# Kernel tuning notes

Hardware: AMD Instinct MI355X
Metric: run time of the kernel (lower is better)

The kernel has to match this reference:

```python
import jax, jax.numpy as jnp
import numpy as np

ALPHA = 1.5
BETA = 45.0
LAMDA = 0.5
B = 8192   # batch_size
D = 128    # feature dim (hardcoded in original via zeros((1,128)))
V = 4      # number of views stacked in fj
EPS = 1e-12  # F.normalize eps


def _l2norm_rows(x):
    n = jnp.sqrt(jnp.sum(x * x, axis=-1, keepdims=True))
    return x / jnp.maximum(n, EPS)


def setup_inputs() -> dict:
    key = jax.random.key(0)
    k1, k2 = jax.random.split(key)
    fi = jax.random.normal(k1, (B, D), dtype=jnp.float32)
    fj = jax.random.normal(k2, (V, B, D), dtype=jnp.float32)
    # L2-normalize embeddings so exp(beta*(SVM - lamda)) stays finite (beta=45)
    fi = _l2norm_rows(fi)
    fj = _l2norm_rows(fj)
    return {"fi": fi, "fj": fj, "b": V}


def avg_svm(fi, fj):
    # Original: per-row softmax-weighted average of fj rows, renormalized,
    # dotted with fi row, averaged over the batch.
    A = fi @ fj.T                      # [B, B] pairwise logits
    W = jax.nn.softmax(A, axis=1)      # softmax over j (alphalist / sumofalpha)
    Vw = W @ fj                        # [B, D] softmax-weighted averages
    Vn = _l2norm_rows(Vw)              # F.normalize(p=2, dim=1)
    return jnp.mean(jnp.sum(fi * Vn, axis=1))  # mean_i fi[i] . Vn[i]


def reference(fi, fj, b):
    b = int(b)
    # SMM1 is recomputed identically every outer iteration in the original;
    # compute once and multiply the per-iteration term by (b-1).
    smm1 = avg_svm(fi, fi)
    if b > 2:
        # inner loop: SMM2sum is a running (cumulative) sum over j=1..b-2,
        # and exp(beta*(SMM2sum - lamda)) is added at every step.
        s_vals = jnp.stack([avg_svm(fi, fj[j]) for j in range(1, b - 1)])
        cum = jnp.cumsum(s_vals)
        ssum = jnp.sum(jnp.exp(BETA * (cum - LAMDA)))
    else:
        ssum = jnp.exp(BETA * (avg_svm(fi, fj) - LAMDA))
    term = (1.0 / ALPHA) * jnp.log1p(jnp.exp(-ALPHA * (smm1 - LAMDA))) \
         + (1.0 / BETA) * jnp.log1p(ssum)
    loss = (b - 1) * term
    return jnp.squeeze(loss)
```

## Files before the change

### kernel.cpp

```cpp
#include <hip/hip_runtime.h>

#define BDIM 8192
#define DDIM 128

typedef __attribute__((ext_vector_type(4))) float floatx4;
typedef __attribute__((ext_vector_type(4))) int   intx4;
typedef __attribute__((ext_vector_type(8))) int   intx8;

#define SLAB (BDIM * DDIM)
#define G8_OFF 64
#define G8T_OFF (64 + 3 * SLAB)

__device__ inline void load_lds16(const void* g, void* l) {
    __builtin_amdgcn_global_load_lds(
        (const __attribute__((address_space(1))) unsigned int*)g,
        (__attribute__((address_space(3))) unsigned int*)l, 16, 0, 0);
}

__device__ inline intx8 ld_pair(const char* base, int c0) {
    union { intx8 v; intx4 h[2]; } u;
    u.h[0] = *(const intx4*)(base + c0 * 16);
    u.h[1] = *(const intx4*)(base + (c0 ^ 1) * 16);
    return u.v;
}

__global__ __launch_bounds__(256)
void prep_kernel(const float* __restrict__ fi, const float* __restrict__ fj,
                 unsigned char* __restrict__ g8, unsigned char* __restrict__ g8T,
                 float* __restrict__ acc)
{
    const int p = blockIdx.y;
    const int kblock = blockIdx.x;
    const int rbase = kblock * 32;
    const int tid = threadIdx.x;
    if (p == 0 && kblock == 0 && tid < 8) acc[tid] = 0.f;
    const float* src = (p == 0) ? fi : (fj + (size_t)p * SLAB);

    __shared__ __align__(16) unsigned char T8[32][144];

    {
        const int row = tid >> 3, c = tid & 7;
        const float* sp = src + (size_t)(rbase + row) * DDIM + c * 16;
        float4 f0 = ((const float4*)sp)[0];
        float4 f1 = ((const float4*)sp)[1];
        float4 f2 = ((const float4*)sp)[2];
        float4 f3 = ((const float4*)sp)[3];
        alignas(16) int w[4];
        w[0] = __builtin_amdgcn_cvt_pk_fp8_f32(f0.x, f0.y, 0, false);
        w[0] = __builtin_amdgcn_cvt_pk_fp8_f32(f0.z, f0.w, w[0], true);
        w[1] = __builtin_amdgcn_cvt_pk_fp8_f32(f1.x, f1.y, 0, false);
        w[1] = __builtin_amdgcn_cvt_pk_fp8_f32(f1.z, f1.w, w[1], true);
        w[2] = __builtin_amdgcn_cvt_pk_fp8_f32(f2.x, f2.y, 0, false);
        w[2] = __builtin_amdgcn_cvt_pk_fp8_f32(f2.z, f2.w, w[2], true);
        w[3] = __builtin_amdgcn_cvt_pk_fp8_f32(f3.x, f3.y, 0, false);
        w[3] = __builtin_amdgcn_cvt_pk_fp8_f32(f3.z, f3.w, w[3], true);
        int4 v = *(int4*)w;
        *(int4*)(g8 + (size_t)p * SLAB + (size_t)(rbase + row) * DDIM + c * 16) = v;
        *(int4*)(&T8[row][c * 16]) = v;
    }
    __syncthreads();
    {
        const int d = tid >> 1, half = tid & 1;
        alignas(16) unsigned char bb[16];
        #pragma unroll
        for (int i = 0; i < 16; ++i) bb[i] = T8[half * 16 + i][d];
        *(int4*)(g8T + (size_t)p * SLAB + (size_t)kblock * 4096 + d * 32 + half * 16) =
            *(int4*)bb;
    }
}

__global__ __launch_bounds__(256, 3)
void flash_kernel(const float* __restrict__ fi,
                  const unsigned char* __restrict__ g8,
                  const unsigned char* __restrict__ g8T,
                  float* __restrict__ acc)
{
    const int b = blockIdx.x;
    const int gp = (b & 7) * 96 + (b >> 3);
    const int p = gp >> 8;
    const int qbase = (gp & 255) * 32;
    const int tid = threadIdx.x;
    const int wave = tid >> 6, lane = tid & 63;
    const int quad = lane >> 4, col = lane & 15;

    __shared__ __align__(16) char smem[37888];
    #define KOFF 0
    #define VOFF 16384
    #define POFF 32768
    #define DOFF 36864
    #define NOFF 37376

    const unsigned char* g8p  = g8  + (size_t)p * SLAB;
    const unsigned char* g8Tp = g8T + (size_t)p * SLAB;

    intx8 qf[2];
    #pragma unroll
    for (int qt = 0; qt < 2; ++qt) {
        const intx4* qp = (const intx4*)(g8 + (size_t)(qbase + qt * 16 + col) * DDIM +
                                         quad * 32);
        union { intx8 v; intx4 h[2]; } u;
        u.h[0] = qp[0];
        u.h[1] = qp[1];
        qf[qt] = u.v;
    }

    floatx4 O[2][2];
    #pragma unroll
    for (int qt = 0; qt < 2; ++qt)
        #pragma unroll
        for (int j = 0; j < 2; ++j)
            O[qt][j] = (floatx4){0.f, 0.f, 0.f, 0.f};

    auto stageK = [&](int kb) {
        #pragma unroll
        for (int i = 0; i < 4; ++i) {
            int s = i * 64 + lane;
            int key = s >> 3, cp = s & 7;
            int c = cp ^ (key & 7);
            const unsigned char* gp8 = g8p +
                (size_t)(kb + wave * 32 + key) * DDIM + c * 16;
            load_lds16(gp8, smem + KOFF + wave * 4096 + i * 1024);
        }
    };
    auto stageV = [&](int kb) {
        #pragma unroll
        for (int i = 0; i < 4; ++i) {
            int s = wave * 256 + i * 64 + lane;
            int d = s >> 3, cp = s & 7;
            int c = cp ^ (d & 7);
            const unsigned char* gp8 = g8Tp +
                (size_t)((kb >> 5) + (c >> 1)) * 4096 + d * 32 + (c & 1) * 16;
            load_lds16(gp8, smem + VOFF + wave * 4096 + i * 1024);
        }
    };

    stageK(0);
    stageV(0);
    __syncthreads();

    for (int k = 0; k < 64; ++k) {
        floatx4 S[2][2];
        #pragma unroll
        for (int kt = 0; kt < 2; ++kt) {
            const int key = kt * 16 + col;
            const int c0 = (quad * 2) ^ (key & 7);
            intx8 kf = ld_pair(smem + KOFF + wave * 4096 + key * 128, c0);
            #pragma unroll
            for (int qt = 0; qt < 2; ++qt)
                S[kt][qt] = __builtin_amdgcn_mfma_scale_f32_16x16x128_f8f6f4(
                    kf, qf[qt], (floatx4){0.f, 0.f, 0.f, 0.f},
                    0, 0,
                    0, 127,
                    0, 127);
        }

        if (k + 1 < 64) stageK((k + 1) * 128);

        #pragma unroll
        for (int kt = 0; kt < 2; ++kt)
            #pragma unroll
            for (int qt = 0; qt < 2; ++qt) {
                int v = __builtin_amdgcn_cvt_pk_fp8_f32(
                    __expf(fminf(S[kt][qt][0], 4.f)),
                    __expf(fminf(S[kt][qt][1], 4.f)), 0, false);
                v = __builtin_amdgcn_cvt_pk_fp8_f32(
                    __expf(fminf(S[kt][qt][2], 4.f)),
                    __expf(fminf(S[kt][qt][3], 4.f)), v, true);
                const int q = qt * 16 + col;
                *(int*)(smem + POFF + q * 128 +
                        (((wave * 2 + kt) ^ (q & 7)) * 16) + quad * 4) = v;
            }

        __syncthreads();

        {
            intx8 vf[2];
            #pragma unroll
            for (int j = 0; j < 2; ++j) {
                const int d = (wave * 2 + j) * 16 + col;
                vf[j] = ld_pair(smem + VOFF + d * 128, (quad * 2) ^ (d & 7));
            }
            #pragma unroll
            for (int qt = 0; qt < 2; ++qt) {
                const int q = qt * 16 + col;
                intx8 pf = ld_pair(smem + POFF + q * 128, (quad * 2) ^ (q & 7));
                #pragma unroll
                for (int j = 0; j < 2; ++j)
                    O[qt][j] = __builtin_amdgcn_mfma_scale_f32_16x16x128_f8f6f4(
                        pf, vf[j], O[qt][j], 0, 0, 0, 127, 0, 127);
            }
        }

        __syncthreads();

        if (k + 1 < 64) stageV((k + 1) * 128);
    }

    float* pdot = (float*)(smem + DOFF);
    float* pnrm = (float*)(smem + NOFF);
    #pragma unroll
    for (int qt = 0; qt < 2; ++qt)
        #pragma unroll
        for (int r = 0; r < 4; ++r) {
            const int q = qt * 16 + quad * 4 + r;
            float dot = 0.f, nr = 0.f;
            #pragma unroll
            for (int j = 0; j < 2; ++j) {
                float o = O[qt][j][r];
                float fq = fi[(size_t)(qbase + q) * DDIM + (wave * 2 + j) * 16 + col];
                dot += fq * o;
                nr += o * o;
            }
            #pragma unroll
            for (int m = 1; m < 16; m <<= 1) {
                dot += __shfl_xor(dot, m, 64);
                nr  += __shfl_xor(nr,  m, 64);
            }
            if (col == 0) {
                pdot[wave * 32 + q] = dot;
                pnrm[wave * 32 + q] = nr;
            }
        }
    __syncthreads();
    if (tid < 32) {
        const int q = tid;
        float D = pdot[q] + pdot[32 + q] + pdot[64 + q] + pdot[96 + q];
        float N = pnrm[q] + pnrm[32 + q] + pnrm[64 + q] + pnrm[96 + q];
        float val = D * rsqrtf(fmaxf(N, 1e-30f));
        #pragma unroll
        for (int m = 1; m < 32; m <<= 1) val += __shfl_xor(val, m, 64);
        if (tid == 0) atomicAdd(&acc[p], val);
    }
}

__global__ void final_kernel(const float* __restrict__ acc, float* __restrict__ out)
{
    if (threadIdx.x == 0 && blockIdx.x == 0) {
        const double s0 = (double)acc[0] / (double)BDIM;
        const double s1 = (double)acc[1] / (double)BDIM;
        const double s2 = (double)acc[2] / (double)BDIM;
        const double t1 = (1.0 / 1.5) * log1p(exp(-1.5 * (s0 - 0.5)));
        const double ssum = exp(45.0 * (s1 - 0.5)) + exp(45.0 * (s1 + s2 - 0.5));
        const double t2 = (1.0 / 45.0) * log1p(ssum);
        out[0] = (float)(3.0 * (t1 + t2));
    }
}

extern "C" void kernel_launch(void* const* d_in, const int* in_sizes, int n_in,
                              void* d_out, int out_size, void* d_ws, size_t ws_size,
                              hipStream_t stream)
{
    const float* fi = (const float*)d_in[0];
    const float* fj = (const float*)d_in[1];

    float* acc = (float*)d_ws;
    unsigned char* g8  = (unsigned char*)d_ws + G8_OFF;
    unsigned char* g8T = (unsigned char*)d_ws + G8T_OFF;

    prep_kernel <<<dim3(BDIM / 32, 3), 256, 0, stream>>>(fi, fj, g8, g8T, acc);
    flash_kernel<<<dim3(768), 256, 0, stream>>>(fi, g8, g8T, acc);
    final_kernel<<<1, 64, 0, stream>>>(acc, (float*)d_out);
}
```

Before: 158.1 us.

## Share K/V tiles across three query groups per 768-thread block with double buffering

The flash kernel is restructured into 256 blocks of 12 waves, with three query groups of four waves each sharing the same K/V tiles staged in LDS. Up to two problem slabs can be staged when a block's queries straddle a slab boundary. K and V are double-buffered and prefetched one iteration ahead using raw s_waitcnt/s_barrier, cutting global-to-LDS traffic and one barrier per iteration. It also drops the fminf clamp before exp. The cost is a large LDS footprint (140 KB), one block per CU, and more complex synchronisation.

```diff
diff --git a/kernel.cpp b/kernel.cpp
--- a/kernel.cpp
+++ b/kernel.cpp
@@ -69,34 +69,41 @@
     }
 }
 
-__global__ __launch_bounds__(256, 3)
+__global__ __launch_bounds__(768)
 void flash_kernel(const float* __restrict__ fi,
                   const unsigned char* __restrict__ g8,
                   const unsigned char* __restrict__ g8T,
                   float* __restrict__ acc)
 {
-    const int b = blockIdx.x;
-    const int gp = (b & 7) * 96 + (b >> 3);
-    const int p = gp >> 8;
-    const int qbase = (gp & 255) * 32;
+    const int bid = blockIdx.x;
+    const int gp = (bid & 7) * 32 + (bid >> 3);
     const int tid = threadIdx.x;
     const int wave = tid >> 6, lane = tid & 63;
+    const int g = wave >> 2, kw = wave & 3;
     const int quad = lane >> 4, col = lane & 15;
 
-    __shared__ __align__(16) char smem[37888];
+    const int qglob = gp * 96 + g * 32;
+    const int pg    = qglob >> 13;
+    const int qloc  = qglob & 8191;
+    const int pA    = (gp * 96) >> 13;
+    const int pB    = (gp * 96 + 64) >> 13;
+    const int need2 = (pB != pA) ? 1 : 0;
+    const int selg  = (pg != pA) ? 1 : 0;
+
+    __shared__ __align__(16) char smem[143360];
     #define KOFF 0
-    #define VOFF 16384
-    #define POFF 32768
-    #define DOFF 36864
-    #define NOFF 37376
-
-    const unsigned char* g8p  = g8  + (size_t)p * SLAB;
-    const unsigned char* g8Tp = g8T + (size_t)p * SLAB;
+    #define VOFF 65536
+    #define POFF 131072
+
+    const unsigned char* kA8 = g8  + (size_t)pA * SLAB;
+    const unsigned char* kB8 = g8  + (size_t)pB * SLAB;
+    const unsigned char* vAT = g8T + (size_t)pA * SLAB;
+    const unsigned char* vBT = g8T + (size_t)pB * SLAB;
 
     intx8 qf[2];
     #pragma unroll
     for (int qt = 0; qt < 2; ++qt) {
-        const intx4* qp = (const intx4*)(g8 + (size_t)(qbase + qt * 16 + col) * DDIM +
+        const intx4* qp = (const intx4*)(g8 + (size_t)(qloc + qt * 16 + col) * DDIM +
                                          quad * 32);
         union { intx8 v; intx4 h[2]; } u;
         u.h[0] = qp[0];
@@ -111,79 +118,91 @@
         for (int j = 0; j < 2; ++j)
             O[qt][j] = (floatx4){0.f, 0.f, 0.f, 0.f};
 
-    auto stageK = [&](int kb) {
-        #pragma unroll
-        for (int i = 0; i < 4; ++i) {
-            int s = i * 64 + lane;
-            int key = s >> 3, cp = s & 7;
-            int c = cp ^ (key & 7);
-            const unsigned char* gp8 = g8p +
-                (size_t)(kb + wave * 32 + key) * DDIM + c * 16;
-            load_lds16(gp8, smem + KOFF + wave * 4096 + i * 1024);
+    auto stageK = [&](int kb, int buf) {
+        for (int s = 0; s <= need2; ++s) {
+            const unsigned char* src = s ? kB8 : kA8;
+            #pragma unroll
+            for (int i = 0; i < 4; ++i) {
+                int t = i * 64 + lane;
+                int keyl = t >> 3, cp = t & 7;
+                int c = cp ^ (keyl & 7);
+                load_lds16(src + (size_t)(kb + wave * 32 + keyl) * DDIM + c * 16,
+                           smem + KOFF + s * 32768 + buf * 16384 +
+                           wave * 4096 + i * 1024);
+            }
         }
     };
-    auto stageV = [&](int kb) {
-        #pragma unroll
-        for (int i = 0; i < 4; ++i) {
-            int s = wave * 256 + i * 64 + lane;
-            int d = s >> 3, cp = s & 7;
-            int c = cp ^ (d & 7);
-            const unsigned char* gp8 = g8Tp +
-                (size_t)((kb >> 5) + (c >> 1)) * 4096 + d * 32 + (c & 1) * 16;
-            load_lds16(gp8, smem + VOFF + wave * 4096 + i * 1024);
+    auto stageV = [&](int kb, int buf) {
+        const int sv = wave - 4;
+        for (int s = 0; s <= need2; ++s) {
+            const unsigned char* src = s ? vBT : vAT;
+            #pragma unroll
+            for (int i = 0; i < 4; ++i) {
+                int t = sv * 256 + i * 64 + lane;
+                int d = t >> 3, cp = t & 7;
+                int c = cp ^ (d & 7);
+                load_lds16(src + (size_t)((kb >> 5) + (c >> 1)) * 4096 +
+                           d * 32 + (c & 1) * 16,
+                           smem + VOFF + s * 32768 + buf * 16384 +
+                           sv * 4096 + i * 1024);
+            }
         }
     };
 
-    stageK(0);
-    stageV(0);
-    __syncthreads();
+    if (wave < 4)      stageK(0, 0);
+    else if (wave < 8) stageV(0, 0);
+    if (wave < 8) asm volatile("s_waitcnt vmcnt(0)" ::: "memory");
+    asm volatile("s_barrier" ::: "memory");
 
     for (int k = 0; k < 64; ++k) {
+        const int buf = k & 1;
+        if (k + 1 < 64) {
+            if (wave < 4)      stageK((k + 1) * 128, buf ^ 1);
+            else if (wave < 8) stageV((k + 1) * 128, buf ^ 1);
+        }
+
+        const char* kbase = smem + KOFF + selg * 32768 + buf * 16384;
         floatx4 S[2][2];
         #pragma unroll
         for (int kt = 0; kt < 2; ++kt) {
-            const int key = kt * 16 + col;
+            const int key = kw * 32 + kt * 16 + col;
             const int c0 = (quad * 2) ^ (key & 7);
-            intx8 kf = ld_pair(smem + KOFF + wave * 4096 + key * 128, c0);
+            intx8 kf = ld_pair(kbase + key * 128, c0);
             #pragma unroll
             for (int qt = 0; qt < 2; ++qt)
                 S[kt][qt] = __builtin_amdgcn_mfma_scale_f32_16x16x128_f8f6f4(
                     kf, qf[qt], (floatx4){0.f, 0.f, 0.f, 0.f},
-                    0, 0,
-                    0, 127,
-                    0, 127);
-        }
-
-        if (k + 1 < 64) stageK((k + 1) * 128);
+                    0, 0, 0, 127, 0, 127);
+        }
 
         #pragma unroll
         for (int kt = 0; kt < 2; ++kt)
             #pragma unroll
             for (int qt = 0; qt < 2; ++qt) {
                 int v = __builtin_amdgcn_cvt_pk_fp8_f32(
-                    __expf(fminf(S[kt][qt][0], 4.f)),
-                    __expf(fminf(S[kt][qt][1], 4.f)), 0, false);
+                    __expf(S[kt][qt][0]), __expf(S[kt][qt][1]), 0, false);
                 v = __builtin_amdgcn_cvt_pk_fp8_f32(
-                    __expf(fminf(S[kt][qt][2], 4.f)),
-                    __expf(fminf(S[kt][qt][3], 4.f)), v, true);
+                    __expf(S[kt][qt][2]), __expf(S[kt][qt][3]), v, true);
                 const int q = qt * 16 + col;
-                *(int*)(smem + POFF + q * 128 +
-                        (((wave * 2 + kt) ^ (q & 7)) * 16) + quad * 4) = v;
-            }
-
-        __syncthreads();
+                *(int*)(smem + POFF + g * 4096 + q * 128 +
+                        (((kw * 2 + kt) ^ (q & 7)) * 16) + quad * 4) = v;
+            }
+
+        asm volatile("s_waitcnt lgkmcnt(0)\n\ts_barrier" ::: "memory");
 
         {
+            const char* vbase = smem + VOFF + selg * 32768 + buf * 16384;
             intx8 vf[2];
             #pragma unroll
             for (int j = 0; j < 2; ++j) {
-                const int d = (wave * 2 + j) * 16 + col;
-                vf[j] = ld_pair(smem + VOFF + d * 128, (quad * 2) ^ (d & 7));
+                const int d = (kw * 2 + j) * 16 + col;
+                vf[j] = ld_pair(vbase + d * 128, (quad * 2) ^ (d & 7));
             }
             #pragma unroll
             for (int qt = 0; qt < 2; ++qt) {
                 const int q = qt * 16 + col;
-                intx8 pf = ld_pair(smem + POFF + q * 128, (quad * 2) ^ (q & 7));
+                intx8 pf = ld_pair(smem + POFF + g * 4096 + q * 128,
+                                   (quad * 2) ^ (q & 7));
                 #pragma unroll
                 for (int j = 0; j < 2; ++j)
                     O[qt][j] = __builtin_amdgcn_mfma_scale_f32_16x16x128_f8f6f4(
@@ -191,13 +210,12 @@
             }
         }
 
-        __syncthreads();
-
-        if (k + 1 < 64) stageV((k + 1) * 128);
-    }
-
-    float* pdot = (float*)(smem + DOFF);
-    float* pnrm = (float*)(smem + NOFF);
+        if (wave < 8) asm volatile("s_waitcnt vmcnt(0)" ::: "memory");
+        asm volatile("s_waitcnt lgkmcnt(0)\n\ts_barrier" ::: "memory");
+    }
+
+    float* pdot = (float*)(smem + POFF + g * 4096);
+    float* pnrm = (float*)(smem + POFF + g * 4096 + 2048);
     #pragma unroll
     for (int qt = 0; qt < 2; ++qt)
         #pragma unroll
@@ -207,7 +225,7 @@
             #pragma unroll
             for (int j = 0; j < 2; ++j) {
                 float o = O[qt][j][r];
-                float fq = fi[(size_t)(qbase + q) * DDIM + (wave * 2 + j) * 16 + col];
+                float fq = fi[(size_t)(qloc + q) * DDIM + (kw * 2 + j) * 16 + col];
                 dot += fq * o;
                 nr += o * o;
             }
@@ -217,19 +235,19 @@
                 nr  += __shfl_xor(nr,  m, 64);
             }
             if (col == 0) {
-                pdot[wave * 32 + q] = dot;
-                pnrm[wave * 32 + q] = nr;
-            }
-        }
-    __syncthreads();
-    if (tid < 32) {
-        const int q = tid;
+                pdot[kw * 32 + q] = dot;
+                pnrm[kw * 32 + q] = nr;
+            }
+        }
+    asm volatile("s_waitcnt lgkmcnt(0)\n\ts_barrier" ::: "memory");
+    if (kw == 0 && lane < 32) {
+        const int q = lane;
         float D = pdot[q] + pdot[32 + q] + pdot[64 + q] + pdot[96 + q];
         float N = pnrm[q] + pnrm[32 + q] + pnrm[64 + q] + pnrm[96 + q];
         float val = D * rsqrtf(fmaxf(N, 1e-30f));
         #pragma unroll
         for (int m = 1; m < 32; m <<= 1) val += __shfl_xor(val, m, 64);
-        if (tid == 0) atomicAdd(&acc[p], val);
+        if (lane == 0) atomicAdd(&acc[pg], val);
     }
 }
 
@@ -258,6 +276,6 @@
     unsigned char* g8T = (unsigned char*)d_ws + G8T_OFF;
 
     prep_kernel <<<dim3(BDIM / 32, 3), 256, 0, stream>>>(fi, fj, g8, g8T, acc);
-    flash_kernel<<<dim3(768), 256, 0, stream>>>(fi, g8, g8T, acc);
+    flash_kernel<<<dim3(256), 768, 0, stream>>>(fi, g8, g8T, acc);
     final_kernel<<<1, 64, 0, stream>>>(acc, (float*)d_out);
 }
```

After: 163.2 us. +3.3%, slower.

## Software-pipeline flash loop with register K, double-buffered V and P

Applied to the files above, without the earlier changes.

Restructures the main loop so K tiles are prefetched straight into registers instead of being staged through LDS. V and the exp'd P tiles are double-buffered in LDS, and the PV product for the previous block runs before the QK product of the current block. This cuts each iteration to a single barrier, so global loads for the next block overlap compute. It also drops the fminf clamp before exp, which is safe only because the inputs are L2-normalized. The costs are more LDS per block and hand-written waitcnt synchronization that must match the load counts exactly.

```diff
diff --git a/kernel.cpp b/kernel.cpp
--- a/kernel.cpp
+++ b/kernel.cpp
@@ -83,12 +83,11 @@
     const int wave = tid >> 6, lane = tid & 63;
     const int quad = lane >> 4, col = lane & 15;
 
-    __shared__ __align__(16) char smem[37888];
-    #define KOFF 0
-    #define VOFF 16384
+    __shared__ __align__(16) char smem[41984];
+    #define VOFF 0
     #define POFF 32768
-    #define DOFF 36864
-    #define NOFF 37376
+    #define DOFF 40960
+    #define NOFF 41472
 
     const unsigned char* g8p  = g8  + (size_t)p * SLAB;
     const unsigned char* g8Tp = g8T + (size_t)p * SLAB;
@@ -111,79 +110,44 @@
         for (int j = 0; j < 2; ++j)
             O[qt][j] = (floatx4){0.f, 0.f, 0.f, 0.f};
 
-    auto stageK = [&](int kb) {
+    auto stageV = [&](int kb, int vbuf) {
         #pragma unroll
         for (int i = 0; i < 4; ++i) {
-            int s = i * 64 + lane;
-            int key = s >> 3, cp = s & 7;
-            int c = cp ^ (key & 7);
-            const unsigned char* gp8 = g8p +
-                (size_t)(kb + wave * 32 + key) * DDIM + c * 16;
-            load_lds16(gp8, smem + KOFF + wave * 4096 + i * 1024);
+            int t = wave * 256 + i * 64 + lane;
+            int d = t >> 3, cp = t & 7;
+            int c = cp ^ (d & 7);
+            load_lds16(g8Tp + (size_t)((kb >> 5) + (c >> 1)) * 4096 +
+                       d * 32 + (c & 1) * 16,
+                       smem + VOFF + vbuf * 16384 + wave * 4096 + i * 1024);
         }
     };
-    auto stageV = [&](int kb) {
-        #pragma unroll
-        for (int i = 0; i < 4; ++i) {
-            int s = wave * 256 + i * 64 + lane;
-            int d = s >> 3, cp = s & 7;
-            int c = cp ^ (d & 7);
-            const unsigned char* gp8 = g8Tp +
-                (size_t)((kb >> 5) + (c >> 1)) * 4096 + d * 32 + (c & 1) * 16;
-            load_lds16(gp8, smem + VOFF + wave * 4096 + i * 1024);
-        }
+    auto loadK = [&](int kb, intx8* kf) {
+        #pragma unroll
+        for (int kt = 0; kt < 2; ++kt)
+            kf[kt] = *(const intx8*)(g8p +
+                (size_t)(kb + wave * 32 + kt * 16 + col) * DDIM + quad * 32);
     };
 
-    stageK(0);
-    stageV(0);
-    __syncthreads();
+    intx8 kfc[2], kfn[2];
+    loadK(0, kfc);
+    stageV(0, 0);
 
     for (int k = 0; k < 64; ++k) {
-        floatx4 S[2][2];
-        #pragma unroll
-        for (int kt = 0; kt < 2; ++kt) {
-            const int key = kt * 16 + col;
-            const int c0 = (quad * 2) ^ (key & 7);
-            intx8 kf = ld_pair(smem + KOFF + wave * 4096 + key * 128, c0);
-            #pragma unroll
-            for (int qt = 0; qt < 2; ++qt)
-                S[kt][qt] = __builtin_amdgcn_mfma_scale_f32_16x16x128_f8f6f4(
-                    kf, qf[qt], (floatx4){0.f, 0.f, 0.f, 0.f},
-                    0, 0,
-                    0, 127,
-                    0, 127);
-        }
-
-        if (k + 1 < 64) stageK((k + 1) * 128);
-
-        #pragma unroll
-        for (int kt = 0; kt < 2; ++kt)
-            #pragma unroll
-            for (int qt = 0; qt < 2; ++qt) {
-                int v = __builtin_amdgcn_cvt_pk_fp8_f32(
-                    __expf(fminf(S[kt][qt][0], 4.f)),
-                    __expf(fminf(S[kt][qt][1], 4.f)), 0, false);
-                v = __builtin_amdgcn_cvt_pk_fp8_f32(
-                    __expf(fminf(S[kt][qt][2], 4.f)),
-                    __expf(fminf(S[kt][qt][3], 4.f)), v, true);
-                const int q = qt * 16 + col;
-                *(int*)(smem + POFF + q * 128 +
-                        (((wave * 2 + kt) ^ (q & 7)) * 16) + quad * 4) = v;
-            }
-
-        __syncthreads();
-
-        {
+        asm volatile("s_waitcnt vmcnt(8)" ::: "memory");
+
+        if (k > 0) {
+            const char* vbase = smem + VOFF + ((k - 1) & 1) * 16384;
+            const char* pbase = smem + POFF + ((k - 1) & 1) * 4096;
             intx8 vf[2];
             #pragma unroll
             for (int j = 0; j < 2; ++j) {
                 const int d = (wave * 2 + j) * 16 + col;
-                vf[j] = ld_pair(smem + VOFF + d * 128, (quad * 2) ^ (d & 7));
+                vf[j] = ld_pair(vbase + d * 128, (quad * 2) ^ (d & 7));
             }
             #pragma unroll
             for (int qt = 0; qt < 2; ++qt) {
                 const int q = qt * 16 + col;
-                intx8 pf = ld_pair(smem + POFF + q * 128, (quad * 2) ^ (q & 7));
+                intx8 pf = ld_pair(pbase + q * 128, (quad * 2) ^ (q & 7));
                 #pragma unroll
                 for (int j = 0; j < 2; ++j)
                     O[qt][j] = __builtin_amdgcn_mfma_scale_f32_16x16x128_f8f6f4(
@@ -191,9 +155,59 @@
             }
         }
 
-        __syncthreads();
-
-        if (k + 1 < 64) stageV((k + 1) * 128);
+        asm volatile("s_waitcnt lgkmcnt(0)" ::: "memory");
+        if (k < 63) {
+            stageV((k + 1) * 128, (k + 1) & 1);
+            loadK((k + 1) * 128, kfn);
+        }
+
+        floatx4 S[2][2];
+        #pragma unroll
+        for (int kt = 0; kt < 2; ++kt)
+            #pragma unroll
+            for (int qt = 0; qt < 2; ++qt)
+                S[kt][qt] = __builtin_amdgcn_mfma_scale_f32_16x16x128_f8f6f4(
+                    kfc[kt], qf[qt], (floatx4){0.f, 0.f, 0.f, 0.f},
+                    0, 0, 0, 127, 0, 127);
+
+        #pragma unroll
+        for (int kt = 0; kt < 2; ++kt)
+            #pragma unroll
+            for (int qt = 0; qt < 2; ++qt) {
+                int v = __builtin_amdgcn_cvt_pk_fp8_f32(
+                    __expf(S[kt][qt][0]), __expf(S[kt][qt][1]), 0, false);
+                v = __builtin_amdgcn_cvt_pk_fp8_f32(
+                    __expf(S[kt][qt][2]), __expf(S[kt][qt][3]), v, true);
+                const int q = qt * 16 + col;
+                *(int*)(smem + POFF + (k & 1) * 4096 + q * 128 +
+                        (((wave * 2 + kt) ^ (q & 7)) * 16) + quad * 4) = v;
+            }
+
+        asm volatile("s_waitcnt lgkmcnt(0)\n\ts_barrier" ::: "memory");
+
+        kfc[0] = kfn[0];
+        kfc[1] = kfn[1];
+    }
+
+    asm volatile("s_waitcnt vmcnt(0)" ::: "memory");
+    {
+        const char* vbase = smem + VOFF + (63 & 1) * 16384;
+        const char* pbase = smem + POFF + (63 & 1) * 4096;
+        intx8 vf[2];
+        #pragma unroll
+        for (int j = 0; j < 2; ++j) {
+            const int d = (wave * 2 + j) * 16 + col;
+            vf[j] = ld_pair(vbase + d * 128, (quad * 2) ^ (d & 7));
+        }
+        #pragma unroll
+        for (int qt = 0; qt < 2; ++qt) {
+            const int q = qt * 16 + col;
+            intx8 pf = ld_pair(pbase + q * 128, (quad * 2) ^ (q & 7));
+            #pragma unroll
+            for (int j = 0; j < 2; ++j)
+                O[qt][j] = __builtin_amdgcn_mfma_scale_f32_16x16x128_f8f6f4(
+                    pf, vf[j], O[qt][j], 0, 0, 0, 127, 0, 127);
+        }
     }
 
     float* pdot = (float*)(smem + DOFF);
```

Result: slower. 208.8 us (+32.1%).

## Replace block barriers with per-wave vmcnt waits and double-buffer P tile

Applied to the files above, without the earlier changes.

Each wave stages only its own K and V slices, so the two full __syncthreads per iteration are replaced by per-wave s_waitcnt vmcnt counting. A single raw s_barrier remains, guarding the P exchange, and P is double-buffered so the next iteration's writes cannot clash with current reads. Global addresses for the staging loads are precomputed and bumped by a pointer increment. MFMA sections are wrapped in s_setprio, and exp now uses a raw exp2 without the clamp to 4, which relies on the normalized inputs keeping the logits small.

```diff
diff --git a/kernel.cpp b/kernel.cpp
--- a/kernel.cpp
+++ b/kernel.cpp
@@ -22,6 +22,10 @@
     u.h[0] = *(const intx4*)(base + c0 * 16);
     u.h[1] = *(const intx4*)(base + (c0 ^ 1) * 16);
     return u.v;
+}
+
+__device__ inline float exp_fast(float x) {
+    return __builtin_amdgcn_exp2f(x * 1.44269504088896341f);
 }
 
 __global__ __launch_bounds__(256)
@@ -83,12 +87,10 @@
     const int wave = tid >> 6, lane = tid & 63;
     const int quad = lane >> 4, col = lane & 15;
 
-    __shared__ __align__(16) char smem[37888];
+    __shared__ __align__(16) char smem[40960];
     #define KOFF 0
     #define VOFF 16384
     #define POFF 32768
-    #define DOFF 36864
-    #define NOFF 37376
 
     const unsigned char* g8p  = g8  + (size_t)p * SLAB;
     const unsigned char* g8Tp = g8T + (size_t)p * SLAB;
@@ -111,35 +113,36 @@
         for (int j = 0; j < 2; ++j)
             O[qt][j] = (floatx4){0.f, 0.f, 0.f, 0.f};
 
-    auto stageK = [&](int kb) {
-        #pragma unroll
-        for (int i = 0; i < 4; ++i) {
-            int s = i * 64 + lane;
-            int key = s >> 3, cp = s & 7;
-            int c = cp ^ (key & 7);
-            const unsigned char* gp8 = g8p +
-                (size_t)(kb + wave * 32 + key) * DDIM + c * 16;
-            load_lds16(gp8, smem + KOFF + wave * 4096 + i * 1024);
-        }
-    };
-    auto stageV = [&](int kb) {
-        #pragma unroll
-        for (int i = 0; i < 4; ++i) {
-            int s = wave * 256 + i * 64 + lane;
-            int d = s >> 3, cp = s & 7;
-            int c = cp ^ (d & 7);
-            const unsigned char* gp8 = g8Tp +
-                (size_t)((kb >> 5) + (c >> 1)) * 4096 + d * 32 + (c & 1) * 16;
-            load_lds16(gp8, smem + VOFF + wave * 4096 + i * 1024);
-        }
-    };
-
-    stageK(0);
-    stageV(0);
-    __syncthreads();
+    const unsigned char* gK[4];
+    const unsigned char* gV[4];
+    #pragma unroll
+    for (int i = 0; i < 4; ++i) {
+        int s = i * 64 + lane;
+        int key = s >> 3, cp = s & 7;
+        int c = cp ^ (key & 7);
+        gK[i] = g8p + (size_t)(wave * 32 + key) * DDIM + c * 16;
+        int t = wave * 256 + i * 64 + lane;
+        int d = t >> 3, cq = t & 7;
+        int cv = cq ^ (d & 7);
+        gV[i] = g8Tp + (size_t)(cv >> 1) * 4096 + d * 32 + (cv & 1) * 16;
+    }
+
+    #pragma unroll
+    for (int i = 0; i < 4; ++i) {
+        load_lds16(gK[i], smem + KOFF + wave * 4096 + i * 1024);
+        gK[i] += 16384;
+    }
+    #pragma unroll
+    for (int i = 0; i < 4; ++i) {
+        load_lds16(gV[i], smem + VOFF + wave * 4096 + i * 1024);
+        gV[i] += 16384;
+    }
 
     for (int k = 0; k < 64; ++k) {
+        asm volatile("s_waitcnt vmcnt(4)" ::: "memory");
+
         floatx4 S[2][2];
+        __builtin_amdgcn_s_setprio(1);
         #pragma unroll
         for (int kt = 0; kt < 2; ++kt) {
             const int key = kt * 16 + col;
@@ -149,31 +152,40 @@
             for (int qt = 0; qt < 2; ++qt)
                 S[kt][qt] = __builtin_amdgcn_mfma_scale_f32_16x16x128_f8f6f4(
                     kf, qf[qt], (floatx4){0.f, 0.f, 0.f, 0.f},
-                    0, 0,
-                    0, 127,
-                    0, 127);
-        }
-
-        if (k + 1 < 64) stageK((k + 1) * 128);
-
+                    0, 0, 0, 127, 0, 127);
+        }
+        __builtin_amdgcn_s_setprio(0);
+
+        asm volatile("s_waitcnt lgkmcnt(0)" ::: "memory");
+        if (k < 63) {
+            #pragma unroll
+            for (int i = 0; i < 4; ++i) {
+                load_lds16(gK[i], smem + KOFF + wave * 4096 + i * 1024);
+                gK[i] += 16384;
+            }
+        }
+
+        char* pw = smem + POFF + ((k & 1) << 12);
         #pragma unroll
         for (int kt = 0; kt < 2; ++kt)
             #pragma unroll
             for (int qt = 0; qt < 2; ++qt) {
                 int v = __builtin_amdgcn_cvt_pk_fp8_f32(
-                    __expf(fminf(S[kt][qt][0], 4.f)),
-                    __expf(fminf(S[kt][qt][1], 4.f)), 0, false);
+                    exp_fast(S[kt][qt][0]), exp_fast(S[kt][qt][1]), 0, false);
                 v = __builtin_amdgcn_cvt_pk_fp8_f32(
-                    __expf(fminf(S[kt][qt][2], 4.f)),
-                    __expf(fminf(S[kt][qt][3], 4.f)), v, true);
+                    exp_fast(S[kt][qt][2]), exp_fast(S[kt][qt][3]), v, true);
                 const int q = qt * 16 + col;
-                *(int*)(smem + POFF + q * 128 +
-                        (((wave * 2 + kt) ^ (q & 7)) * 16) + quad * 4) = v;
-            }
-
-        __syncthreads();
-
+                *(int*)(pw + q * 128 +
+                        (((wave * 2 + kt) ^ (q & 7)) << 4) + quad * 4) = v;
+            }
+
+        asm volatile("s_waitcnt lgkmcnt(0)\n\ts_barrier" ::: "memory");
+
+        asm volatile("s_waitcnt vmcnt(4)" ::: "memory");
+
+        __builtin_amdgcn_s_setprio(1);
         {
+            const char* pr = smem + POFF + ((k & 1) << 12);
             intx8 vf[2];
             #pragma unroll
             for (int j = 0; j < 2; ++j) {
@@ -183,21 +195,27 @@
             #pragma unroll
             for (int qt = 0; qt < 2; ++qt) {
                 const int q = qt * 16 + col;
-                intx8 pf = ld_pair(smem + POFF + q * 128, (quad * 2) ^ (q & 7));
+                intx8 pf = ld_pair(pr + q * 128, (quad * 2) ^ (q & 7));
                 #pragma unroll
                 for (int j = 0; j < 2; ++j)
                     O[qt][j] = __builtin_amdgcn_mfma_scale_f32_16x16x128_f8f6f4(
                         pf, vf[j], O[qt][j], 0, 0, 0, 127, 0, 127);
             }
         }
-
-        __syncthreads();
-
-        if (k + 1 < 64) stageV((k + 1) * 128);
-    }
-
-    float* pdot = (float*)(smem + DOFF);
-    float* pnrm = (float*)(smem + NOFF);
+        __builtin_amdgcn_s_setprio(0);
+
+        asm volatile("s_waitcnt lgkmcnt(0)" ::: "memory");
+        if (k < 63) {
+            #pragma unroll
+            for (int i = 0; i < 4; ++i) {
+                load_lds16(gV[i], smem + VOFF + wave * 4096 + i * 1024);
+                gV[i] += 16384;
+            }
+        }
+    }
+
+    float* pdot = (float*)(smem + POFF);
+    float* pnrm = (float*)(smem + POFF + 512);
     #pragma unroll
     for (int qt = 0; qt < 2; ++qt)
         #pragma unroll
```

Measured after the change: 154.8 us. 1.02x faster.
